# Kernel optimization log

Measured on AMD Instinct MI355X. Metric: run time of the kernel, lower is better.

## Reference

```python
import jax, jax.numpy as jnp
import numpy as np
import math

NUM_GRIDS = 128
INPUT_DIM = 128
OUTPUT_DIM = 128
BATCH = 8192
INIT_SCALE = 0.1


def _borders_cdf_grid(n_chunks):
    # inverse Laplace CDF grid borders, exactly as in the torch module
    def inv(u):
        return np.log(2.0 * u) if u <= 0.5 else -np.log(2.0 * (1.0 - u))
    cs = 1.0 / n_chunks
    b = [inv(i * cs) for i in range(1, n_chunks)]
    left = b[0] - (b[1] - b[0])
    right = b[-1] + (b[-1] - b[-2])
    return np.array([left] + b + [right], dtype=np.float32)  # [n_chunks+1]


def setup_inputs() -> dict:
    key = jax.random.key(0)
    kx, kp = jax.random.split(key)
    x = jax.random.normal(kx, (INPUT_DIM, BATCH), dtype=jnp.float32)
    s = INIT_SCALE / math.sqrt(INPUT_DIM)
    func_parameter = jax.random.uniform(
        kp, (NUM_GRIDS + 1, OUTPUT_DIM, INPUT_DIM), dtype=jnp.float32,
        minval=-s, maxval=s)
    borders = jnp.asarray(_borders_cdf_grid(NUM_GRIDS))
    inverse_chunk_lengths = 1.0 / (borders[1:] - borders[:-1])  # [NUM_GRIDS]
    return {"x": x, "func_parameter": func_parameter,
            "borders": borders, "inverse_chunk_lengths": inverse_chunk_lengths}


def reference(x, func_parameter, borders, inverse_chunk_lengths):
    # x: [I, B]; func_parameter: [G+1, O, I]
    G = borders.shape[0] - 1
    I = x.shape[0]
    # Laplace CDF: R -> [0, 1]
    exp_na = jnp.exp(-jnp.abs(x))
    cdf = jnp.where(x > 0, 1.0 - 0.5 * exp_na, 0.5 * exp_na)
    # bucketize on uniform CDF grid (truncation == floor since cdf*G >= 0)
    idx = jnp.clip((cdf * G).astype(jnp.int32), 0, G - 1)        # [I, B]
    idx_next = jnp.clip(idx + 1, 0, G)                           # [I, B]
    left = borders[idx]                                          # [I, B]
    inv_len = inverse_chunk_lengths[idx]                         # [I, B]
    d = (x - left) * inv_len                                     # [I, B]
    # gather per-input-dim parameter rows: val[i, b, o] = P[idx[i,b], o, i]
    Pt = jnp.transpose(func_parameter, (2, 0, 1))                # [I, G+1, O]
    rows = jnp.arange(I)[:, None]                                # [I, 1]
    val_l = Pt[rows, idx]                                        # [I, B, O]
    val_r = Pt[rows, idx_next]                                   # [I, B, O]
    out = ((1.0 - d)[..., None] * val_l + d[..., None] * val_r).sum(axis=0)  # [B, O]
    return out.T                                                 # [O, B]
```

## Files before the change

### kernel.cpp

```cpp
#include <hip/hip_runtime.h>
#include <cstdint>


#define NG 128
#define NI 128
#define NO 128
#define NB 8192
#define WO 4
#define PH 8

using half2v = __attribute__((ext_vector_type(2))) _Float16;
using float4v = __attribute__((ext_vector_type(4))) float;

__device__ inline uint32_t pack_f16x2(float lo, float hi) {
    _Float16 hl = (_Float16)lo, hh = (_Float16)hi;
    return (uint32_t)__builtin_bit_cast(unsigned short, hl) |
           ((uint32_t)__builtin_bit_cast(unsigned short, hh) << 16);
}

__global__ __launch_bounds__(256) void build_q(const float* __restrict__ P,
                                               uint32_t* __restrict__ Q2) {
    __shared__ float L[5][16][128];
    const int gb = blockIdx.x >> 3;
    const int ob = blockIdx.x & 7;
    const int g0 = gb * 4;
    const int o0 = ob * 16;
    const int s0 = ob * 4;
    const int t  = threadIdx.x;
    #pragma unroll
    for (int pass = 0; pass < 40; ++pass) {
        int row = pass * 2 + (t >> 7);
        int i   = t & 127;
        int gg  = row >> 4, ol = row & 15;
        L[gg][ol][i] = P[(size_t)(g0 + gg) * (NO * NI) + (o0 + ol) * NI + i];
    }
    __syncthreads();
    #pragma unroll
    for (int pp = 0; pp < 2; ++pp) {
        int item = pp * 256 + t;
        int i  = item & 127;
        int sl = item >> 7;
        uint32_t* dst = Q2 + ((size_t)((s0 + sl) * NI + i) * NG + g0) * 4;
        #pragma unroll
        for (int gg = 0; gg < 4; ++gg) {
            uint32_t r[4];
            #pragma unroll
            for (int ow = 0; ow < 4; ++ow) {
                float pl = L[gg][sl * 4 + ow][i];
                float dd = L[gg + 1][sl * 4 + ow][i] - pl;
                r[ow] = pack_f16x2(pl, dd);
            }
            *(uint4*)(dst + gg * 4) = make_uint4(r[0], r[1], r[2], r[3]);
        }
    }
}

__global__ __launch_bounds__(256) void build_t(const float* __restrict__ x,
                                               const float* __restrict__ borders,
                                               const float* __restrict__ icl,
                                               uint32_t* __restrict__ T) {
    const int e0 = (blockIdx.x * 256 + threadIdx.x) * 4;
    const float4 xv = *(const float4*)(x + e0);
    uint32_t r[4];
    const float xs[4] = {xv.x, xv.y, xv.z, xv.w};
    #pragma unroll
    for (int k = 0; k < 4; ++k) {
        float v = xs[k];
        float ea = __expf(-fabsf(v));
        float cdf = v > 0.f ? 1.f - 0.5f * ea : 0.5f * ea;
        int idx = (int)(cdf * 128.f);
        idx = idx > 127 ? 127 : idx;
        float d = (v - borders[idx]) * icl[idx];
        _Float16 hd = (_Float16)d;
        r[k] = ((uint32_t)idx << 4) |
               ((uint32_t)__builtin_bit_cast(unsigned short, hd) << 16);
    }
    *(uint4*)(T + e0) = make_uint4(r[0], r[1], r[2], r[3]);
}

__global__ __launch_bounds__(1024, 8) void main_k(const uint32_t* __restrict__ Q2,
                                                  const uint32_t* __restrict__ T,
                                                  float* __restrict__ part) {
    __shared__ uint32_t slab[2][PH][NG * WO];
    const int t    = threadIdx.x;
    const int bx   = blockIdx.x;
    const int s    = bx & 31;
    const int ih   = (bx >> 5) & 1;
    const int bblk = (bx >> 6) << 10;
    const int bme  = bblk + t;
    const uint32_t* Qs = Q2 + ((size_t)s * NI + ih * 64) * (NG * WO);
    const uint32_t* Ts = T + (size_t)(ih * 64) * NB;

    float a0 = 0.f, a1 = 0.f, a2 = 0.f, a3 = 0.f;

    uint32_t treg[PH];
    {
        uint4 q0 = *(const uint4*)(Qs + (size_t)t * 4);
        #pragma unroll
        for (int il = 0; il < PH; ++il)
            treg[il] = Ts[(size_t)il * NB + bme];
        ((uint4*)&slab[0][0][0])[t] = q0;
    }
    __syncthreads();

    #pragma unroll
    for (int p = 0; p < 8; ++p) {
        const int cur = p & 1;
        uint32_t tnxt[PH];
        uint4 qnxt;
        if (p < 7) {
            qnxt = *(const uint4*)(Qs + (size_t)(p + 1) * (PH * NG * WO) +
                                   (size_t)t * 4);
            #pragma unroll
            for (int il = 0; il < PH; ++il)
                tnxt[il] = Ts[(size_t)((p + 1) * PH + il) * NB + bme];
        }
        #pragma unroll
        for (int il = 0; il < PH; ++il) {
            uint32_t tw  = treg[il];
            uint32_t off = tw & 0xFFFFu;
            uint32_t w2b = (tw & 0xFFFF0000u) | 0x3C00u;
            uint4 q = *(const uint4*)((const char*)&slab[cur][il][0] + off);
            half2v w2 = __builtin_bit_cast(half2v, w2b);
            a0 = __builtin_amdgcn_fdot2(__builtin_bit_cast(half2v, q.x), w2, a0, false);
            a1 = __builtin_amdgcn_fdot2(__builtin_bit_cast(half2v, q.y), w2, a1, false);
            a2 = __builtin_amdgcn_fdot2(__builtin_bit_cast(half2v, q.z), w2, a2, false);
            a3 = __builtin_amdgcn_fdot2(__builtin_bit_cast(half2v, q.w), w2, a3, false);
        }
        if (p < 7) {
            ((uint4*)&slab[cur ^ 1][0][0])[t] = qnxt;
            #pragma unroll
            for (int il = 0; il < PH; ++il)
                treg[il] = tnxt[il];
            __syncthreads();
        }
    }

    float* po = part + (size_t)ih * (NO * NB) + (size_t)(s * 4) * NB + bme;
    __builtin_nontemporal_store(a0, po);
    __builtin_nontemporal_store(a1, po + NB);
    __builtin_nontemporal_store(a2, po + 2 * (size_t)NB);
    __builtin_nontemporal_store(a3, po + 3 * (size_t)NB);
}

__global__ __launch_bounds__(256) void reduce_k(const float* __restrict__ part,
                                                float* __restrict__ out) {
    const int e0 = (blockIdx.x * 256 + threadIdx.x) * 4;
    const float4v v0 = *(const float4v*)(part + e0);
    const float4v v1 = *(const float4v*)(part + (size_t)NO * NB + e0);
    const float4v r = v0 + v1;
    __builtin_nontemporal_store(r, (float4v*)(out + e0));
}

extern "C" void kernel_launch(void* const* d_in, const int* in_sizes, int n_in,
                              void* d_out, int out_size, void* d_ws, size_t ws_size,
                              hipStream_t stream) {
    const float* x       = (const float*)d_in[0];
    const float* P       = (const float*)d_in[1];
    const float* borders = (const float*)d_in[2];
    const float* icl     = (const float*)d_in[3];
    float* out = (float*)d_out;

    uint32_t* Q2 = (uint32_t*)d_ws;
    uint32_t* T  = Q2 + (size_t)NO * NI * NG;
    float*    prt = (float*)(T + (size_t)NI * NB);

    hipLaunchKernelGGL(build_q, dim3(256), dim3(256), 0, stream, P, Q2);
    hipLaunchKernelGGL(build_t, dim3(NI * NB / 1024), dim3(256), 0, stream,
                       x, borders, icl, T);
    hipLaunchKernelGGL(main_k, dim3(512), dim3(1024), 0, stream, Q2, T, prt);
    hipLaunchKernelGGL(reduce_k, dim3(NO * NB / 1024), dim3(256), 0, stream,
                       prt, out);
}
```

Baseline: 92.58 us.

## Fuse build kernels, transpose T layout, remap blocks across XCDs, shrink main blocks

Merges build_q and build_t into one launch, with the T build transposing through shared memory so each batch element's indices for all inputs are contiguous. main_k then loads them as two vector loads per phase instead of eight strided loads. main_k moves to 512-thread blocks with block indices swizzled so blocks sharing Q slabs and T rows land on the same XCD, and reduce_k uses a matching mapping. The partial stores become regular stores instead of nontemporal ones. Cost: more shared memory per build block, plus a transpose step.

```diff
diff --git a/kernel.cpp b/kernel.cpp
--- a/kernel.cpp
+++ b/kernel.cpp
@@ -9,7 +9,7 @@
 #define WO 4
 #define PH 8
 
-using half2v = __attribute__((ext_vector_type(2))) _Float16;
+using half2v  = __attribute__((ext_vector_type(2))) _Float16;
 using float4v = __attribute__((ext_vector_type(4))) float;
 
 __device__ inline uint32_t pack_f16x2(float lo, float hi) {
@@ -18,109 +18,127 @@
            ((uint32_t)__builtin_bit_cast(unsigned short, hh) << 16);
 }
 
-__global__ __launch_bounds__(256) void build_q(const float* __restrict__ P,
-                                               uint32_t* __restrict__ Q2) {
-    __shared__ float L[5][16][128];
-    const int gb = blockIdx.x >> 3;
-    const int ob = blockIdx.x & 7;
-    const int g0 = gb * 4;
-    const int o0 = ob * 16;
-    const int s0 = ob * 4;
-    const int t  = threadIdx.x;
-    #pragma unroll
-    for (int pass = 0; pass < 40; ++pass) {
-        int row = pass * 2 + (t >> 7);
-        int i   = t & 127;
-        int gg  = row >> 4, ol = row & 15;
-        L[gg][ol][i] = P[(size_t)(g0 + gg) * (NO * NI) + (o0 + ol) * NI + i];
-    }
-    __syncthreads();
-    #pragma unroll
-    for (int pp = 0; pp < 2; ++pp) {
-        int item = pp * 256 + t;
-        int i  = item & 127;
-        int sl = item >> 7;
-        uint32_t* dst = Q2 + ((size_t)((s0 + sl) * NI + i) * NG + g0) * 4;
+__global__ __launch_bounds__(256) void build_k(const float* __restrict__ P,
+                                               const float* __restrict__ x,
+                                               const float* __restrict__ borders,
+                                               const float* __restrict__ icl,
+                                               uint32_t* __restrict__ Q2,
+                                               uint32_t* __restrict__ T2) {
+    __shared__ __align__(16) char smem[40960];
+    const int t = threadIdx.x;
+    if (blockIdx.x < 256) {
+        float (*L)[16][128] = (float (*)[16][128])smem;
+        const int gb = blockIdx.x >> 3;
+        const int ob = blockIdx.x & 7;
+        const int g0 = gb * 4, o0 = ob * 16, s0 = ob * 4;
         #pragma unroll
-        for (int gg = 0; gg < 4; ++gg) {
-            uint32_t r[4];
+        for (int pass = 0; pass < 40; ++pass) {
+            int row = pass * 2 + (t >> 7);
+            int i   = t & 127;
+            int gg  = row >> 4, ol = row & 15;
+            L[gg][ol][i] = P[(size_t)(g0 + gg) * (NO * NI) + (o0 + ol) * NI + i];
+        }
+        __syncthreads();
+        #pragma unroll
+        for (int pp = 0; pp < 2; ++pp) {
+            int item = pp * 256 + t;
+            int i  = item & 127;
+            int sl = item >> 7;
+            uint32_t* dst = Q2 + ((size_t)((s0 + sl) * NI + i) * NG + g0) * 4;
             #pragma unroll
-            for (int ow = 0; ow < 4; ++ow) {
-                float pl = L[gg][sl * 4 + ow][i];
-                float dd = L[gg + 1][sl * 4 + ow][i] - pl;
-                r[ow] = pack_f16x2(pl, dd);
+            for (int gg = 0; gg < 4; ++gg) {
+                uint32_t r[4];
+                #pragma unroll
+                for (int ow = 0; ow < 4; ++ow) {
+                    float pl = L[gg][sl * 4 + ow][i];
+                    float dd = L[gg + 1][sl * 4 + ow][i] - pl;
+                    r[ow] = pack_f16x2(pl, dd);
+                }
+                *(uint4*)(dst + gg * 4) = make_uint4(r[0], r[1], r[2], r[3]);
             }
-            *(uint4*)(dst + gg * 4) = make_uint4(r[0], r[1], r[2], r[3]);
+        }
+    } else {
+        uint32_t (*Lt)[65] = (uint32_t (*)[65])smem;
+        const int b0 = (blockIdx.x - 256) * 64;
+        #pragma unroll
+        for (int f = 0; f < 8; ++f) {
+            int q  = f * 256 + t;
+            int i  = q >> 4;
+            int c4 = (q & 15) * 4;
+            const float4 xv = *(const float4*)(x + (size_t)i * NB + b0 + c4);
+            const float xs[4] = {xv.x, xv.y, xv.z, xv.w};
+            #pragma unroll
+            for (int j = 0; j < 4; ++j) {
+                float v = xs[j];
+                float ea = __expf(-fabsf(v));
+                float cdf = v > 0.f ? 1.f - 0.5f * ea : 0.5f * ea;
+                int idx = (int)(cdf * 128.f);
+                idx = idx > 127 ? 127 : idx;
+                float d = (v - borders[idx]) * icl[idx];
+                _Float16 hd = (_Float16)d;
+                Lt[i][c4 + j] = ((uint32_t)idx << 4) |
+                                ((uint32_t)__builtin_bit_cast(unsigned short, hd) << 16);
+            }
+        }
+        __syncthreads();
+        #pragma unroll
+        for (int k = 0; k < 8; ++k) {
+            int flat = t * 4 + k * 1024;
+            int bl = flat >> 7;
+            int i0 = flat & 127;
+            uint4 r = make_uint4(Lt[i0][bl], Lt[i0 + 1][bl],
+                                 Lt[i0 + 2][bl], Lt[i0 + 3][bl]);
+            *(uint4*)(T2 + (size_t)(b0 + bl) * NI + i0) = r;
         }
     }
 }
 
-__global__ __launch_bounds__(256) void build_t(const float* __restrict__ x,
-                                               const float* __restrict__ borders,
-                                               const float* __restrict__ icl,
-                                               uint32_t* __restrict__ T) {
-    const int e0 = (blockIdx.x * 256 + threadIdx.x) * 4;
-    const float4 xv = *(const float4*)(x + e0);
-    uint32_t r[4];
-    const float xs[4] = {xv.x, xv.y, xv.z, xv.w};
-    #pragma unroll
-    for (int k = 0; k < 4; ++k) {
-        float v = xs[k];
-        float ea = __expf(-fabsf(v));
-        float cdf = v > 0.f ? 1.f - 0.5f * ea : 0.5f * ea;
-        int idx = (int)(cdf * 128.f);
-        idx = idx > 127 ? 127 : idx;
-        float d = (v - borders[idx]) * icl[idx];
-        _Float16 hd = (_Float16)d;
-        r[k] = ((uint32_t)idx << 4) |
-               ((uint32_t)__builtin_bit_cast(unsigned short, hd) << 16);
-    }
-    *(uint4*)(T + e0) = make_uint4(r[0], r[1], r[2], r[3]);
-}
-
-__global__ __launch_bounds__(1024, 8) void main_k(const uint32_t* __restrict__ Q2,
-                                                  const uint32_t* __restrict__ T,
-                                                  float* __restrict__ part) {
-    __shared__ uint32_t slab[2][PH][NG * WO];
+__global__ __launch_bounds__(512, 8) void main_k(const uint32_t* __restrict__ Q2,
+                                                 const uint32_t* __restrict__ T2,
+                                                 float* __restrict__ part) {
+    __shared__ __align__(16) uint32_t slab[2][PH][512];
     const int t    = threadIdx.x;
     const int bx   = blockIdx.x;
-    const int s    = bx & 31;
-    const int ih   = (bx >> 5) & 1;
-    const int bblk = (bx >> 6) << 10;
-    const int bme  = bblk + t;
+    const int xcd  = bx & 7;
+    const int rest = bx >> 3;
+    const int s    = ((rest & 7) << 2) | (xcd & 3);
+    const int ih   = (rest >> 3) & 1;
+    const int bt   = (((rest >> 4) & 7) << 1) | (xcd >> 2);
+    const int bme  = (bt << 9) | t;
     const uint32_t* Qs = Q2 + ((size_t)s * NI + ih * 64) * (NG * WO);
-    const uint32_t* Ts = T + (size_t)(ih * 64) * NB;
+    const uint32_t* Tr = T2 + (size_t)bme * NI + ih * 64;
 
     float a0 = 0.f, a1 = 0.f, a2 = 0.f, a3 = 0.f;
 
-    uint32_t treg[PH];
+    uint4 ta = *(const uint4*)(Tr);
+    uint4 tb = *(const uint4*)(Tr + 4);
     {
-        uint4 q0 = *(const uint4*)(Qs + (size_t)t * 4);
-        #pragma unroll
-        for (int il = 0; il < PH; ++il)
-            treg[il] = Ts[(size_t)il * NB + bme];
-        ((uint4*)&slab[0][0][0])[t] = q0;
+        uint4 qa = *(const uint4*)(Qs + (size_t)t * 4);
+        uint4 qb = *(const uint4*)(Qs + 2048 + (size_t)t * 4);
+        ((uint4*)&slab[0][0][0])[t]       = qa;
+        ((uint4*)&slab[0][0][0])[t + 512] = qb;
     }
     __syncthreads();
 
     #pragma unroll
     for (int p = 0; p < 8; ++p) {
         const int cur = p & 1;
-        uint32_t tnxt[PH];
-        uint4 qnxt;
+        uint4 qna, qnb, tna, tnb;
         if (p < 7) {
-            qnxt = *(const uint4*)(Qs + (size_t)(p + 1) * (PH * NG * WO) +
-                                   (size_t)t * 4);
-            #pragma unroll
-            for (int il = 0; il < PH; ++il)
-                tnxt[il] = Ts[(size_t)((p + 1) * PH + il) * NB + bme];
+            const uint32_t* qsrc = Qs + (size_t)(p + 1) * 4096;
+            qna = *(const uint4*)(qsrc + (size_t)t * 4);
+            qnb = *(const uint4*)(qsrc + 2048 + (size_t)t * 4);
+            tna = *(const uint4*)(Tr + (p + 1) * 8);
+            tnb = *(const uint4*)(Tr + (p + 1) * 8 + 4);
         }
+        const char* sp = (const char*)&slab[cur][0][0];
+        const uint32_t tc[8] = {ta.x, ta.y, ta.z, ta.w, tb.x, tb.y, tb.z, tb.w};
         #pragma unroll
         for (int il = 0; il < PH; ++il) {
-            uint32_t tw  = treg[il];
+            uint32_t tw  = tc[il];
             uint32_t off = tw & 0xFFFFu;
             uint32_t w2b = (tw & 0xFFFF0000u) | 0x3C00u;
-            uint4 q = *(const uint4*)((const char*)&slab[cur][il][0] + off);
+            uint4 q = *(const uint4*)(sp + il * 2048 + off);
             half2v w2 = __builtin_bit_cast(half2v, w2b);
             a0 = __builtin_amdgcn_fdot2(__builtin_bit_cast(half2v, q.x), w2, a0, false);
             a1 = __builtin_amdgcn_fdot2(__builtin_bit_cast(half2v, q.y), w2, a1, false);
@@ -128,27 +146,34 @@
             a3 = __builtin_amdgcn_fdot2(__builtin_bit_cast(half2v, q.w), w2, a3, false);
         }
         if (p < 7) {
-            ((uint4*)&slab[cur ^ 1][0][0])[t] = qnxt;
-            #pragma unroll
-            for (int il = 0; il < PH; ++il)
-                treg[il] = tnxt[il];
+            ((uint4*)&slab[cur ^ 1][0][0])[t]       = qna;
+            ((uint4*)&slab[cur ^ 1][0][0])[t + 512] = qnb;
+            ta = tna; tb = tnb;
             __syncthreads();
         }
     }
 
     float* po = part + (size_t)ih * (NO * NB) + (size_t)(s * 4) * NB + bme;
-    __builtin_nontemporal_store(a0, po);
-    __builtin_nontemporal_store(a1, po + NB);
-    __builtin_nontemporal_store(a2, po + 2 * (size_t)NB);
-    __builtin_nontemporal_store(a3, po + 3 * (size_t)NB);
+    po[0]                = a0;
+    po[NB]               = a1;
+    po[2 * (size_t)NB]   = a2;
+    po[3 * (size_t)NB]   = a3;
 }
 
-__global__ __launch_bounds__(256) void reduce_k(const float* __restrict__ part,
+__global__ __launch_bounds__(128) void reduce_k(const float* __restrict__ part,
                                                 float* __restrict__ out) {
-    const int e0 = (blockIdx.x * 256 + threadIdx.x) * 4;
+    const int rb   = blockIdx.x;
+    const int xcd  = rb & 7;
+    const int rest = rb >> 3;
+    const int olo  = rest & 3;
+    const int ohi  = (rest >> 2) & 7;
+    const int bthi = (rest >> 5) & 7;
+    const int o    = (ohi << 4) | ((xcd & 3) << 2) | olo;
+    const int bt   = (bthi << 1) | (xcd >> 2);
+    const int e0   = o * NB + bt * 512 + threadIdx.x * 4;
     const float4v v0 = *(const float4v*)(part + e0);
     const float4v v1 = *(const float4v*)(part + (size_t)NO * NB + e0);
-    const float4v r = v0 + v1;
+    const float4v r  = v0 + v1;
     __builtin_nontemporal_store(r, (float4v*)(out + e0));
 }
 
@@ -161,14 +186,12 @@
     const float* icl     = (const float*)d_in[3];
     float* out = (float*)d_out;
 
-    uint32_t* Q2 = (uint32_t*)d_ws;
-    uint32_t* T  = Q2 + (size_t)NO * NI * NG;
-    float*    prt = (float*)(T + (size_t)NI * NB);
+    uint32_t* Q2  = (uint32_t*)d_ws;
+    uint32_t* T2  = Q2 + (size_t)NO * NI * NG;
+    float*    prt = (float*)(T2 + (size_t)NI * NB);
 
-    hipLaunchKernelGGL(build_q, dim3(256), dim3(256), 0, stream, P, Q2);
-    hipLaunchKernelGGL(build_t, dim3(NI * NB / 1024), dim3(256), 0, stream,
-                       x, borders, icl, T);
-    hipLaunchKernelGGL(main_k, dim3(512), dim3(1024), 0, stream, Q2, T, prt);
-    hipLaunchKernelGGL(reduce_k, dim3(NO * NB / 1024), dim3(256), 0, stream,
-                       prt, out);
+    hipLaunchKernelGGL(build_k, dim3(384), dim3(256), 0, stream,
+                       P, x, borders, icl, Q2, T2);
+    hipLaunchKernelGGL(main_k, dim3(1024), dim3(512), 0, stream, Q2, T2, prt);
+    hipLaunchKernelGGL(reduce_k, dim3(2048), dim3(128), 0, stream, prt, out);
 }
```

After: 124.9 us. 34.9% more time.

## Drop input-dim split and reduce kernel; triple-buffer Q via direct global-to-LDS loads

Applied to the files above, without the earlier changes.

The main kernel now has each block cover all 128 input dims over 16 phases, instead of splitting them across two blocks. It writes final outputs directly, so the partial buffer and the separate reduce kernel are gone. Q slabs are loaded straight into LDS with global_load_lds into a three-slot ring two phases ahead, using manual waitcnt and raw barriers. This removes the reduce launch and the partial-sum traffic. The cost is half as many blocks (256), which lowers parallelism and per-CU occupancy, and fragile hand-written wait counts.

```diff
diff --git a/kernel.cpp b/kernel.cpp
--- a/kernel.cpp
+++ b/kernel.cpp
@@ -6,16 +6,21 @@
 #define NI 128
 #define NO 128
 #define NB 8192
-#define WO 4
 #define PH 8
+#define NPH 16
 
 using half2v = __attribute__((ext_vector_type(2))) _Float16;
-using float4v = __attribute__((ext_vector_type(4))) float;
 
 __device__ inline uint32_t pack_f16x2(float lo, float hi) {
     _Float16 hl = (_Float16)lo, hh = (_Float16)hi;
     return (uint32_t)__builtin_bit_cast(unsigned short, hl) |
            ((uint32_t)__builtin_bit_cast(unsigned short, hh) << 16);
+}
+
+__device__ inline void load_lds16(const uint32_t* g, uint32_t* l) {
+    __builtin_amdgcn_global_load_lds(
+        (const __attribute__((address_space(1))) uint32_t*)g,
+        (__attribute__((address_space(3))) uint32_t*)l, 16, 0, 0);
 }
 
 __global__ __launch_bounds__(256) void build_q(const float* __restrict__ P,
@@ -78,78 +83,74 @@
     *(uint4*)(T + e0) = make_uint4(r[0], r[1], r[2], r[3]);
 }
 
-__global__ __launch_bounds__(1024, 8) void main_k(const uint32_t* __restrict__ Q2,
-                                                  const uint32_t* __restrict__ T,
-                                                  float* __restrict__ part) {
-    __shared__ uint32_t slab[2][PH][NG * WO];
-    const int t    = threadIdx.x;
-    const int bx   = blockIdx.x;
-    const int s    = bx & 31;
-    const int ih   = (bx >> 5) & 1;
-    const int bblk = (bx >> 6) << 10;
-    const int bme  = bblk + t;
-    const uint32_t* Qs = Q2 + ((size_t)s * NI + ih * 64) * (NG * WO);
-    const uint32_t* Ts = T + (size_t)(ih * 64) * NB;
+__global__ __launch_bounds__(1024) void main_k(const uint32_t* __restrict__ Q2,
+                                               const uint32_t* __restrict__ T,
+                                               float* __restrict__ out) {
+    __shared__ __align__(16) uint32_t slab[3][PH * NG * 4];
+    const int t   = threadIdx.x;
+    const int bx  = blockIdx.x;
+    const int s   = bx & 31;
+    const int bt  = bx >> 5;
+    const int bme = (bt << 10) | t;
+    const uint32_t* Qs = Q2 + (size_t)s * (NI * NG * 4);
 
     float a0 = 0.f, a1 = 0.f, a2 = 0.f, a3 = 0.f;
 
-    uint32_t treg[PH];
-    {
-        uint4 q0 = *(const uint4*)(Qs + (size_t)t * 4);
-        #pragma unroll
-        for (int il = 0; il < PH; ++il)
-            treg[il] = Ts[(size_t)il * NB + bme];
-        ((uint4*)&slab[0][0][0])[t] = q0;
-    }
-    __syncthreads();
+    uint32_t tc[PH];
+    #pragma unroll
+    for (int il = 0; il < PH; ++il)
+        tc[il] = T[(size_t)il * NB + bme];
+    asm volatile("" ::: "memory");
+    load_lds16(Qs + (size_t)t * 4,                  &slab[0][t * 4]);
+    load_lds16(Qs + (size_t)(PH * NG * 4) + t * 4,  &slab[1][t * 4]);
+    asm volatile("s_waitcnt vmcnt(1)" ::: "memory");
+    __builtin_amdgcn_s_barrier();
+    __builtin_amdgcn_sched_barrier(0);
 
     #pragma unroll
-    for (int p = 0; p < 8; ++p) {
-        const int cur = p & 1;
-        uint32_t tnxt[PH];
-        uint4 qnxt;
-        if (p < 7) {
-            qnxt = *(const uint4*)(Qs + (size_t)(p + 1) * (PH * NG * WO) +
-                                   (size_t)t * 4);
+    for (int p = 0; p < NPH; ++p) {
+        uint32_t tn[PH];
+        if (p < NPH - 1) {
             #pragma unroll
             for (int il = 0; il < PH; ++il)
-                tnxt[il] = Ts[(size_t)((p + 1) * PH + il) * NB + bme];
+                tn[il] = T[(size_t)((p + 1) * PH + il) * NB + bme];
         }
+        asm volatile("" ::: "memory");
+        if (p < NPH - 2) {
+            load_lds16(Qs + (size_t)(p + 2) * (PH * NG * 4) + t * 4,
+                       &slab[(p + 2) % 3][t * 4]);
+        }
+        const char* sp = (const char*)&slab[p % 3][0];
         #pragma unroll
         for (int il = 0; il < PH; ++il) {
-            uint32_t tw  = treg[il];
+            uint32_t tw  = tc[il];
             uint32_t off = tw & 0xFFFFu;
             uint32_t w2b = (tw & 0xFFFF0000u) | 0x3C00u;
-            uint4 q = *(const uint4*)((const char*)&slab[cur][il][0] + off);
+            uint4 q = *(const uint4*)(sp + il * 2048 + off);
             half2v w2 = __builtin_bit_cast(half2v, w2b);
             a0 = __builtin_amdgcn_fdot2(__builtin_bit_cast(half2v, q.x), w2, a0, false);
             a1 = __builtin_amdgcn_fdot2(__builtin_bit_cast(half2v, q.y), w2, a1, false);
             a2 = __builtin_amdgcn_fdot2(__builtin_bit_cast(half2v, q.z), w2, a2, false);
             a3 = __builtin_amdgcn_fdot2(__builtin_bit_cast(half2v, q.w), w2, a3, false);
         }
-        if (p < 7) {
-            ((uint4*)&slab[cur ^ 1][0][0])[t] = qnxt;
+        if (p < NPH - 1) {
             #pragma unroll
             for (int il = 0; il < PH; ++il)
-                treg[il] = tnxt[il];
-            __syncthreads();
+                tc[il] = tn[il];
+            if (p < NPH - 2)
+                asm volatile("s_waitcnt vmcnt(1) lgkmcnt(0)" ::: "memory");
+            else
+                asm volatile("s_waitcnt vmcnt(0) lgkmcnt(0)" ::: "memory");
+            __builtin_amdgcn_s_barrier();
+            __builtin_amdgcn_sched_barrier(0);
         }
     }
 
-    float* po = part + (size_t)ih * (NO * NB) + (size_t)(s * 4) * NB + bme;
-    __builtin_nontemporal_store(a0, po);
-    __builtin_nontemporal_store(a1, po + NB);
-    __builtin_nontemporal_store(a2, po + 2 * (size_t)NB);
-    __builtin_nontemporal_store(a3, po + 3 * (size_t)NB);
-}
-
-__global__ __launch_bounds__(256) void reduce_k(const float* __restrict__ part,
-                                                float* __restrict__ out) {
-    const int e0 = (blockIdx.x * 256 + threadIdx.x) * 4;
-    const float4v v0 = *(const float4v*)(part + e0);
-    const float4v v1 = *(const float4v*)(part + (size_t)NO * NB + e0);
-    const float4v r = v0 + v1;
-    __builtin_nontemporal_store(r, (float4v*)(out + e0));
+    size_t ob = (size_t)(s * 4) * NB + bme;
+    __builtin_nontemporal_store(a0, out + ob);
+    __builtin_nontemporal_store(a1, out + ob + NB);
+    __builtin_nontemporal_store(a2, out + ob + 2 * (size_t)NB);
+    __builtin_nontemporal_store(a3, out + ob + 3 * (size_t)NB);
 }
 
 extern "C" void kernel_launch(void* const* d_in, const int* in_sizes, int n_in,
@@ -163,12 +164,9 @@
 
     uint32_t* Q2 = (uint32_t*)d_ws;
     uint32_t* T  = Q2 + (size_t)NO * NI * NG;
-    float*    prt = (float*)(T + (size_t)NI * NB);
 
     hipLaunchKernelGGL(build_q, dim3(256), dim3(256), 0, stream, P, Q2);
     hipLaunchKernelGGL(build_t, dim3(NI * NB / 1024), dim3(256), 0, stream,
                        x, borders, icl, T);
-    hipLaunchKernelGGL(main_k, dim3(512), dim3(1024), 0, stream, Q2, T, prt);
-    hipLaunchKernelGGL(reduce_k, dim3(NO * NB / 1024), dim3(256), 0, stream,
-                       prt, out);
+    hipLaunchKernelGGL(main_k, dim3(256), dim3(1024), 0, stream, Q2, T, out);
 }
```

Result: slower. 327.8 us (+254.0%).

## Stage full Q slab once via direct global-to-LDS loads and reuse across batch

Applied to the files above, without the earlier changes.

The main kernel now loads the block's entire 128KB parameter slab (64 inputs x 128 grids x 4 outputs) into LDS once, using global_load_lds, instead of double-buffering 8-input phases with a barrier per phase. Each block then processes two batch chunks of 1024 columns against that slab, with register prefetch of T in groups of 16. This halves the grid to 256 blocks and removes repeated Q loads and syncs. The trade-off is lower occupancy from the large LDS footprint, with at most one block per CU, and the initial load is not overlapped with compute. Partial stores become regular rather than nontemporal.

```diff
diff --git a/kernel.cpp b/kernel.cpp
--- a/kernel.cpp
+++ b/kernel.cpp
@@ -6,16 +6,20 @@
 #define NI 128
 #define NO 128
 #define NB 8192
-#define WO 4
-#define PH 8
 
-using half2v = __attribute__((ext_vector_type(2))) _Float16;
+using half2v  = __attribute__((ext_vector_type(2))) _Float16;
 using float4v = __attribute__((ext_vector_type(4))) float;
 
 __device__ inline uint32_t pack_f16x2(float lo, float hi) {
     _Float16 hl = (_Float16)lo, hh = (_Float16)hi;
     return (uint32_t)__builtin_bit_cast(unsigned short, hl) |
            ((uint32_t)__builtin_bit_cast(unsigned short, hh) << 16);
+}
+
+__device__ inline void load_lds16(const uint32_t* g, uint32_t* l) {
+    __builtin_amdgcn_global_load_lds(
+        (const __attribute__((address_space(1))) uint32_t*)g,
+        (__attribute__((address_space(3))) uint32_t*)l, 16, 0, 0);
 }
 
 __global__ __launch_bounds__(256) void build_q(const float* __restrict__ P,
@@ -78,69 +82,65 @@
     *(uint4*)(T + e0) = make_uint4(r[0], r[1], r[2], r[3]);
 }
 
-__global__ __launch_bounds__(1024, 8) void main_k(const uint32_t* __restrict__ Q2,
+__global__ __launch_bounds__(1024, 4) void main_k(const uint32_t* __restrict__ Q2,
                                                   const uint32_t* __restrict__ T,
                                                   float* __restrict__ part) {
-    __shared__ uint32_t slab[2][PH][NG * WO];
-    const int t    = threadIdx.x;
-    const int bx   = blockIdx.x;
-    const int s    = bx & 31;
-    const int ih   = (bx >> 5) & 1;
-    const int bblk = (bx >> 6) << 10;
-    const int bme  = bblk + t;
-    const uint32_t* Qs = Q2 + ((size_t)s * NI + ih * 64) * (NG * WO);
-    const uint32_t* Ts = T + (size_t)(ih * 64) * NB;
+    __shared__ __align__(16) uint32_t slab[64 * NG * 4];
+    const int t   = threadIdx.x;
+    const int bx  = blockIdx.x;
+    const int win = bx & 7;
+    const int s   = bx >> 3;
+    const int ih  = win >> 2;
+    const int bq  = win & 3;
+    const uint32_t* Qs = Q2 + ((size_t)s * NI + ih * 64) * (NG * 4);
 
-    float a0 = 0.f, a1 = 0.f, a2 = 0.f, a3 = 0.f;
-
-    uint32_t treg[PH];
-    {
-        uint4 q0 = *(const uint4*)(Qs + (size_t)t * 4);
-        #pragma unroll
-        for (int il = 0; il < PH; ++il)
-            treg[il] = Ts[(size_t)il * NB + bme];
-        ((uint4*)&slab[0][0][0])[t] = q0;
-    }
+    #pragma unroll
+    for (int k = 0; k < 8; ++k)
+        load_lds16(Qs + (size_t)(t + k * 1024) * 4, &slab[(t + k * 1024) * 4]);
     __syncthreads();
 
     #pragma unroll
-    for (int p = 0; p < 8; ++p) {
-        const int cur = p & 1;
-        uint32_t tnxt[PH];
-        uint4 qnxt;
-        if (p < 7) {
-            qnxt = *(const uint4*)(Qs + (size_t)(p + 1) * (PH * NG * WO) +
-                                   (size_t)t * 4);
+    for (int bb = 0; bb < 2; ++bb) {
+        const int bcol = (bq << 11) + (bb << 10) + t;
+        const uint32_t* Tb = T + (size_t)(ih * 64) * NB + bcol;
+        float a0 = 0.f, a1 = 0.f, a2 = 0.f, a3 = 0.f;
+        uint32_t tt[16];
+        #pragma unroll
+        for (int il = 0; il < 16; ++il)
+            tt[il] = Tb[(size_t)il * NB];
+        #pragma unroll
+        for (int ic = 0; ic < 4; ++ic) {
+            uint32_t tn[16];
+            if (ic < 3) {
+                #pragma unroll
+                for (int il = 0; il < 16; ++il)
+                    tn[il] = Tb[(size_t)((ic + 1) * 16 + il) * NB];
+            }
+            const char* sp = (const char*)slab + ic * 32768;
             #pragma unroll
-            for (int il = 0; il < PH; ++il)
-                tnxt[il] = Ts[(size_t)((p + 1) * PH + il) * NB + bme];
+            for (int il = 0; il < 16; ++il) {
+                uint32_t tw  = tt[il];
+                uint32_t off = tw & 0xFFFFu;
+                uint32_t w2b = (tw & 0xFFFF0000u) | 0x3C00u;
+                uint4 q = *(const uint4*)(sp + il * 2048 + off);
+                half2v w2 = __builtin_bit_cast(half2v, w2b);
+                a0 = __builtin_amdgcn_fdot2(__builtin_bit_cast(half2v, q.x), w2, a0, false);
+                a1 = __builtin_amdgcn_fdot2(__builtin_bit_cast(half2v, q.y), w2, a1, false);
+                a2 = __builtin_amdgcn_fdot2(__builtin_bit_cast(half2v, q.z), w2, a2, false);
+                a3 = __builtin_amdgcn_fdot2(__builtin_bit_cast(half2v, q.w), w2, a3, false);
+            }
+            if (ic < 3) {
+                #pragma unroll
+                for (int il = 0; il < 16; ++il)
+                    tt[il] = tn[il];
+            }
         }
-        #pragma unroll
-        for (int il = 0; il < PH; ++il) {
-            uint32_t tw  = treg[il];
-            uint32_t off = tw & 0xFFFFu;
-            uint32_t w2b = (tw & 0xFFFF0000u) | 0x3C00u;
-            uint4 q = *(const uint4*)((const char*)&slab[cur][il][0] + off);
-            half2v w2 = __builtin_bit_cast(half2v, w2b);
-            a0 = __builtin_amdgcn_fdot2(__builtin_bit_cast(half2v, q.x), w2, a0, false);
-            a1 = __builtin_amdgcn_fdot2(__builtin_bit_cast(half2v, q.y), w2, a1, false);
-            a2 = __builtin_amdgcn_fdot2(__builtin_bit_cast(half2v, q.z), w2, a2, false);
-            a3 = __builtin_amdgcn_fdot2(__builtin_bit_cast(half2v, q.w), w2, a3, false);
-        }
-        if (p < 7) {
-            ((uint4*)&slab[cur ^ 1][0][0])[t] = qnxt;
-            #pragma unroll
-            for (int il = 0; il < PH; ++il)
-                treg[il] = tnxt[il];
-            __syncthreads();
-        }
+        float* po = part + (size_t)ih * (NO * NB) + (size_t)(s * 4) * NB + bcol;
+        po[0]              = a0;
+        po[NB]             = a1;
+        po[2 * (size_t)NB] = a2;
+        po[3 * (size_t)NB] = a3;
     }
-
-    float* po = part + (size_t)ih * (NO * NB) + (size_t)(s * 4) * NB + bme;
-    __builtin_nontemporal_store(a0, po);
-    __builtin_nontemporal_store(a1, po + NB);
-    __builtin_nontemporal_store(a2, po + 2 * (size_t)NB);
-    __builtin_nontemporal_store(a3, po + 3 * (size_t)NB);
 }
 
 __global__ __launch_bounds__(256) void reduce_k(const float* __restrict__ part,
@@ -148,7 +148,7 @@
     const int e0 = (blockIdx.x * 256 + threadIdx.x) * 4;
     const float4v v0 = *(const float4v*)(part + e0);
     const float4v v1 = *(const float4v*)(part + (size_t)NO * NB + e0);
-    const float4v r = v0 + v1;
+    const float4v r  = v0 + v1;
     __builtin_nontemporal_store(r, (float4v*)(out + e0));
 }
 
@@ -161,14 +161,14 @@
     const float* icl     = (const float*)d_in[3];
     float* out = (float*)d_out;
 
-    uint32_t* Q2 = (uint32_t*)d_ws;
-    uint32_t* T  = Q2 + (size_t)NO * NI * NG;
+    uint32_t* Q2  = (uint32_t*)d_ws;
+    uint32_t* T   = Q2 + (size_t)NO * NI * NG;
     float*    prt = (float*)(T + (size_t)NI * NB);
 
     hipLaunchKernelGGL(build_q, dim3(256), dim3(256), 0, stream, P, Q2);
     hipLaunchKernelGGL(build_t, dim3(NI * NB / 1024), dim3(256), 0, stream,
                        x, borders, icl, T);
-    hipLaunchKernelGGL(main_k, dim3(512), dim3(1024), 0, stream, Q2, T, prt);
+    hipLaunchKernelGGL(main_k, dim3(256), dim3(1024), 0, stream, Q2, T, prt);
     hipLaunchKernelGGL(reduce_k, dim3(NO * NB / 1024), dim3(256), 0, stream,
                        prt, out);
 }
```

New measurement: 108.6 us. 1.17x slower.
